# Kernel tuning notes

Measured on AMD Instinct MI355X. Metric: run time of the kernel, lower is better.

Reference implementation:

```python
import jax, jax.numpy as jnp
import numpy as np

CODEBOOK_SIZE = 32768
EMBED_DIM = 4


def setup_inputs() -> dict:
    key = jax.random.key(0)
    k1, k2 = jax.random.split(key)
    # [batch, temporal, channels, height, width]
    hidden_state = jax.random.normal(k1, (1, 4, EMBED_DIM, 48, 48), dtype=jnp.float32)
    # nn.Embedding weight, init uniform(-1/cb, 1/cb) as in the torch module
    embedding = jax.random.uniform(
        k2, (CODEBOOK_SIZE, EMBED_DIM), dtype=jnp.float32,
        minval=-1.0 / CODEBOOK_SIZE, maxval=1.0 / CODEBOOK_SIZE,
    )
    return {"hidden_state": hidden_state, "embedding": embedding}


def reference(hidden_state, embedding):
    b, t, c, h, w = hidden_state.shape
    # permute channels last, flatten to [N, C]
    x = jnp.transpose(hidden_state, (0, 1, 3, 4, 2)).reshape(-1, c)
    distances = (
        jnp.sum(x * x, axis=1, keepdims=True)
        + jnp.sum(embedding * embedding, axis=1)
        - 2.0 * jnp.einsum("nd,kd->nk", x, embedding)
    )
    min_encoding_indices = jnp.argmin(distances, axis=1)
    return min_encoding_indices.reshape(b, t, h, w)
```

## Files before the change

kernel.cpp:

```cpp
#include <hip/hip_runtime.h>
#include <cfloat>


#define ROWS  12
#define BLOCK 512
#define WAVES (BLOCK / 64)
#define NROWS 9216
#define NK    32768
#define EPT   2
#define CHUNK (BLOCK * EPT)

__device__ __forceinline__ float rlf(float v) {
    return __builtin_bit_cast(float,
        __builtin_amdgcn_readfirstlane(__builtin_bit_cast(int, v)));
}

__global__ __launch_bounds__(256)
void vq_prep(const float4* __restrict__ cb, float* __restrict__ e2t)
{
    int k = blockIdx.x * 256 + threadIdx.x;
    float4 e = cb[k];
    e2t[k] = __fadd_rn(__fadd_rn(__fadd_rn(__fmul_rn(e.x, e.x),
                                           __fmul_rn(e.y, e.y)),
                                 __fmul_rn(e.z, e.z)),
                       __fmul_rn(e.w, e.w));
}

__global__ __launch_bounds__(BLOCK)
__attribute__((amdgpu_waves_per_eu(3, 4)))
void vq_argmin_kernel(const float* __restrict__ hs,
                      const float4* __restrict__ cb,
                      const float* __restrict__ e2t,
                      int* __restrict__ out)
{
    __shared__ float sRD[WAVES * ROWS];
    __shared__ int   sRI[WAVES * ROWS];

    const int tid = threadIdx.x;
    const int rowbase = blockIdx.x * ROWS;

    float sx0[ROWS], sx1[ROWS], sx2[ROWS], sx3[ROWS], sq[ROWS];
    float best[ROWS];
    int   bidx[ROWS];

    #pragma unroll
    for (int r = 0; r < ROWS; ++r) {
        int n = rowbase + r;
        int t = n / 2304;
        int rem = n - t * 2304;
        const float* ptr = hs + t * 9216 + rem;
        float a0 = ptr[0], a1 = ptr[2304], a2 = ptr[4608], a3 = ptr[6912];
        float q = __fadd_rn(__fadd_rn(__fadd_rn(__fmul_rn(a0, a0),
                                                __fmul_rn(a1, a1)),
                                      __fmul_rn(a2, a2)),
                            __fmul_rn(a3, a3));
        sx0[r] = rlf(a0); sx1[r] = rlf(a1);
        sx2[r] = rlf(a2); sx3[r] = rlf(a3);
        sq[r]  = rlf(q);
        best[r] = FLT_MAX; bidx[r] = 0;
    }

    float4 eA[EPT], eB[EPT];
    float  qA[EPT], qB[EPT];

    auto load_chunk = [&](float4* e, float* q, int tb) {
        #pragma unroll
        for (int j = 0; j < EPT; ++j) {
            e[j] = cb[tb + tid + j * BLOCK];
            q[j] = e2t[tb + tid + j * BLOCK];
        }
    };
    auto compute_chunk = [&](const float4* e, const float* q, int tb) {
        float4 ea = e[0], eb = e[1];
        float  qa = q[0], qb = q[1];
        int m1 = tb / BLOCK;
        int m2 = m1 + 1;
        #pragma unroll
        for (int r = 0; r < ROWS; ++r) {
            float dota = __fmul_rn(sx0[r], ea.x);
            dota = __fmaf_rn(sx1[r], ea.y, dota);
            dota = __fmaf_rn(sx2[r], ea.z, dota);
            dota = __fmaf_rn(sx3[r], ea.w, dota);
            float ta = __fadd_rn(sq[r], qa);
            float da = __fmaf_rn(dota, -2.0f, ta);

            float dotb = __fmul_rn(sx0[r], eb.x);
            dotb = __fmaf_rn(sx1[r], eb.y, dotb);
            dotb = __fmaf_rn(sx2[r], eb.z, dotb);
            dotb = __fmaf_rn(sx3[r], eb.w, dotb);
            float tb2 = __fadd_rn(sq[r], qb);
            float db = __fmaf_rn(dotb, -2.0f, tb2);

            float nb = fminf(fminf(best[r], da), db);
            int   w  = (da <= db) ? m1 : m2;
            if (nb < best[r]) bidx[r] = w;
            best[r] = nb;
        }
    };

    load_chunk(eA, qA, 0);
    for (int tb = 0; tb < NK; tb += 2 * CHUNK) {
        load_chunk(eB, qB, tb + CHUNK);
        compute_chunk(eA, qA, tb);
        int nb2 = tb + 2 * CHUNK < NK ? tb + 2 * CHUNK : 0;
        load_chunk(eA, qA, nb2);
        compute_chunk(eB, qB, tb + CHUNK);
    }

    int kk[ROWS];
    #pragma unroll
    for (int r = 0; r < ROWS; ++r) kk[r] = bidx[r] * BLOCK + tid;

    #pragma unroll
    for (int r = 0; r < ROWS; ++r) {
        float d = best[r]; int i = kk[r];
        #pragma unroll
        for (int off = 32; off >= 1; off >>= 1) {
            float d2 = __shfl_xor(d, off, 64);
            int   i2 = __shfl_xor(i, off, 64);
            if (d2 < d || (d2 == d && i2 < i)) { d = d2; i = i2; }
        }
        best[r] = d; kk[r] = i;
    }

    int wave = tid >> 6;
    if ((tid & 63) == 0) {
        #pragma unroll
        for (int r = 0; r < ROWS; ++r) {
            sRD[wave * ROWS + r] = best[r];
            sRI[wave * ROWS + r] = kk[r];
        }
    }
    __syncthreads();

    if (tid < ROWS) {
        float d = sRD[tid]; int i = sRI[tid];
        #pragma unroll
        for (int w = 1; w < WAVES; ++w) {
            float d2 = sRD[w * ROWS + tid];
            int   i2 = sRI[w * ROWS + tid];
            if (d2 < d || (d2 == d && i2 < i)) { d = d2; i = i2; }
        }
        out[rowbase + tid] = i;
    }
}

extern "C" void kernel_launch(void* const* d_in, const int* in_sizes, int n_in,
                              void* d_out, int out_size, void* d_ws, size_t ws_size,
                              hipStream_t stream)
{
    const float*  hs = (const float*)d_in[0];
    const float4* cb = (const float4*)d_in[1];
    int* out = (int*)d_out;

    float* e2t = (float*)d_ws;

    vq_prep<<<NK / 256, 256, 0, stream>>>(cb, e2t);

    dim3 grid(NROWS / ROWS), block(BLOCK);
    vq_argmin_kernel<<<grid, block, 0, stream>>>(hs, cb, e2t, out);
}
```

Before: 119.5 us.

## Split codebook search across two blocks and merge with packed 64-bit atomicMin

```diff
diff --git a/kernel.cpp b/kernel.cpp
--- a/kernel.cpp
+++ b/kernel.cpp
@@ -2,13 +2,16 @@
 #include <cfloat>
 
 
-#define ROWS  12
-#define BLOCK 512
-#define WAVES (BLOCK / 64)
-#define NROWS 9216
-#define NK    32768
-#define EPT   2
-#define CHUNK (BLOCK * EPT)
+#define ROWS   12
+#define BLOCK  512
+#define WAVES  (BLOCK / 64)
+#define NROWS  9216
+#define NRG    (NROWS / ROWS)
+#define KSPLIT 2
+#define NK     32768
+#define NSEG   (NK / KSPLIT)
+#define EPT    2
+#define CHUNK  (BLOCK * EPT)
 
 __device__ __forceinline__ float rlf(float v) {
     return __builtin_bit_cast(float,
@@ -16,7 +19,8 @@
 }
 
 __global__ __launch_bounds__(256)
-void vq_prep(const float4* __restrict__ cb, float* __restrict__ e2t)
+void vq_prep(const float4* __restrict__ cb, float* __restrict__ e2t,
+             unsigned long long* __restrict__ keys)
 {
     int k = blockIdx.x * 256 + threadIdx.x;
     float4 e = cb[k];
@@ -24,20 +28,24 @@
                                            __fmul_rn(e.y, e.y)),
                                  __fmul_rn(e.z, e.z)),
                        __fmul_rn(e.w, e.w));
+    if (k < NROWS) keys[k] = ~0ull;
 }
 
 __global__ __launch_bounds__(BLOCK)
-__attribute__((amdgpu_waves_per_eu(3, 4)))
+__attribute__((amdgpu_waves_per_eu(4, 8)))
 void vq_argmin_kernel(const float* __restrict__ hs,
                       const float4* __restrict__ cb,
                       const float* __restrict__ e2t,
-                      int* __restrict__ out)
+                      unsigned long long* __restrict__ keys)
 {
     __shared__ float sRD[WAVES * ROWS];
     __shared__ int   sRI[WAVES * ROWS];
 
-    const int tid = threadIdx.x;
-    const int rowbase = blockIdx.x * ROWS;
+    const int tid  = threadIdx.x;
+    const int rg   = blockIdx.x % NRG;
+    const int seg  = blockIdx.x / NRG;
+    const int rowbase = rg * ROWS;
+    const int base    = seg * NSEG;
 
     float sx0[ROWS], sx1[ROWS], sx2[ROWS], sx3[ROWS], sq[ROWS];
     float best[ROWS];
@@ -98,11 +106,11 @@
         }
     };
 
-    load_chunk(eA, qA, 0);
-    for (int tb = 0; tb < NK; tb += 2 * CHUNK) {
+    load_chunk(eA, qA, base);
+    for (int tb = base; tb < base + NSEG; tb += 2 * CHUNK) {
         load_chunk(eB, qB, tb + CHUNK);
         compute_chunk(eA, qA, tb);
-        int nb2 = tb + 2 * CHUNK < NK ? tb + 2 * CHUNK : 0;
+        int nb2 = tb + 2 * CHUNK < base + NSEG ? tb + 2 * CHUNK : base;
         load_chunk(eA, qA, nb2);
         compute_chunk(eB, qB, tb + CHUNK);
     }
@@ -141,8 +149,19 @@
             int   i2 = sRI[w * ROWS + tid];
             if (d2 < d || (d2 == d && i2 < i)) { d = d2; i = i2; }
         }
-        out[rowbase + tid] = i;
+        unsigned long long key =
+            ((unsigned long long)__builtin_bit_cast(unsigned, d) << 32) |
+            (unsigned)i;
+        atomicMin(keys + rowbase + tid, key);
     }
+}
+
+__global__ __launch_bounds__(256)
+void vq_extract(const unsigned long long* __restrict__ keys,
+                int* __restrict__ out)
+{
+    int n = blockIdx.x * 256 + threadIdx.x;
+    out[n] = (int)(keys[n] & 0xFFFFFFFFull);
 }
 
 extern "C" void kernel_launch(void* const* d_in, const int* in_sizes, int n_in,
@@ -153,10 +172,13 @@
     const float4* cb = (const float4*)d_in[1];
     int* out = (int*)d_out;
 
-    float* e2t = (float*)d_ws;
+    unsigned long long* keys = (unsigned long long*)d_ws;
+    float* e2t = (float*)((char*)d_ws + NROWS * sizeof(unsigned long long));
 
-    vq_prep<<<NK / 256, 256, 0, stream>>>(cb, e2t);
+    vq_prep<<<NK / 256, 256, 0, stream>>>(cb, e2t, keys);
 
-    dim3 grid(NROWS / ROWS), block(BLOCK);
-    vq_argmin_kernel<<<grid, block, 0, stream>>>(hs, cb, e2t, out);
+    dim3 grid(NRG * KSPLIT), block(BLOCK);
+    vq_argmin_kernel<<<grid, block, 0, stream>>>(hs, cb, e2t, keys);
+
+    vq_extract<<<NROWS / 256, 256, 0, stream>>>(keys, out);
 }
```

After: 127.8 us. +6.9%, slower.
